# Performance work log

Measured on AMD Instinct MI355X. Metric: run time of the kernel, lower is better.

The kernel has to match this reference:

```python
import jax, jax.numpy as jnp
import numpy as np


def _nearest(x, h, w):
    # torch F.interpolate(mode='nearest'): src_idx = floor(dst_idx * in/out)
    Hi, Wi = x.shape[-2], x.shape[-1]
    ri = (jnp.arange(h) * Hi) // h
    ci = (jnp.arange(w) * Wi) // w
    return jnp.take(jnp.take(x, ri, axis=-2), ci, axis=-1)


def _conv2d(x, wgt, bias):
    y = jax.lax.conv_general_dilated(x, wgt, (1, 1), 'SAME',
                                     dimension_numbers=('NCHW', 'OIHW', 'NCHW'))
    return y + bias.reshape(1, -1, 1, 1)


def setup_inputs() -> dict:
    key = jax.random.key(0)
    ks = jax.random.split(key, 6)
    b, c, ref_n, h, w = 1, 128, 4, 64, 64
    Hv, Wv = 256, 256
    return {
        'feats_t': jax.random.normal(ks[0], (b, c, h, w), jnp.float32),
        'feats_ref': jax.random.normal(ks[1], (b, c, ref_n, h, w), jnp.float32),
        'v_t': jax.random.uniform(ks[2], (b, 1, Hv, Wv), dtype=jnp.float32),
        'v_ref': jax.random.uniform(ks[3], (b, 1, ref_n, Hv, Wv), dtype=jnp.float32),
        'conv1_w': jax.random.normal(ks[4], (1, 1, 3, 3), jnp.float32) * 0.1,
        'conv1_b': jnp.zeros((1,), jnp.float32),
        'conv2_w': jax.random.normal(ks[5], (1, 1, 3, 3), jnp.float32) * 0.1,
        'conv2_b': jnp.zeros((1,), jnp.float32),
    }


def reference(feats_t, feats_ref, v_t, v_ref, conv1_w, conv1_b, conv2_w, conv2_b):
    b, c, ref_n, h, w = feats_ref.shape
    # nearest-resize visibility masks to feature resolution
    vt = _nearest(v_t, h, w)                      # (b, 1, h, w)
    vr = _nearest(v_ref, h, w)                    # (b, 1, ref_n, h, w)
    ft = feats_t * vt                             # (b, c, h, w)
    fr = feats_ref * vr                           # (b, c, ref_n, h, w)
    # cost volume: corr[b,r,q,k] = sum_c ft[b,c,q] * fr[b,c,r,k]
    corr = jnp.einsum('bcq,bcrk->brqk',
                      ft.reshape(b, c, h * w),
                      fr.reshape(b, c, ref_n, h * w))
    corr = corr.reshape(b, ref_n, h, w, h, w)
    # separable 4D conv: 3x3 over (h_ref, w_ref), then 3x3 over (h_t, w_t)
    x = _conv2d(corr.reshape(b * ref_n * h * w, 1, h, w), conv1_w, conv1_b)
    x = x.reshape(b, ref_n, h, w, h, w).transpose(0, 1, 4, 5, 2, 3)
    x = _conv2d(x.reshape(b * ref_n * h * w, 1, h, w), conv2_w, conv2_b)
    corr = x.reshape(b, ref_n, h, w, h, w).transpose(0, 1, 4, 5, 2, 3)
    # softmax3d: joint softmax over (ref_n, h_ref, w_ref) per query location
    m = jnp.max(corr, axis=(1, 4, 5), keepdims=True)
    e = jnp.exp(corr - m)
    corr = e / jnp.sum(e, axis=(1, 4, 5), keepdims=True)
    # weighted aggregation: out[b,c,q] = sum_{r,k} fr[b,c,r,k] * corr[b,r,q,k]
    out = jnp.einsum('bcrk,brqk->bcq',
                     fr.reshape(b, c, ref_n, h * w),
                     corr.reshape(b, ref_n, h * w, h * w))
    return out.reshape(b, c, h, w)
```

## Files before the change

kernel.cpp:

```cpp
#include <hip/hip_runtime.h>
#include <stdint.h>

typedef short bf16x8 __attribute__((ext_vector_type(8)));
typedef float f32x16 __attribute__((ext_vector_type(16)));
typedef unsigned int uint4v __attribute__((ext_vector_type(4)));

#define GAS __attribute__((address_space(1)))
#define LAS __attribute__((address_space(3)))

#define CDIM 128
#define NQ   4096
#define NK   16384
#define QT   128
#define KTILE 64

__device__ __forceinline__ unsigned short f2bf(float f) {
    unsigned int u = __builtin_bit_cast(unsigned int, f);
    u = (u + 0x7fffu + ((u >> 16) & 1u)) >> 16;
    return (unsigned short)u;
}

__device__ __forceinline__ void gload_lds16(const void* g, void* l) {
    __builtin_amdgcn_global_load_lds((const GAS unsigned int*)g, (LAS unsigned int*)l, 16, 0, 0);
}

__device__ __forceinline__ unsigned cvtpk(float a, float b) {
    unsigned r;
    asm("v_cvt_pk_bf16_f32 %0, %1, %2" : "=v"(r) : "v"(a), "v"(b));
    return r;
}

__device__ __forceinline__ void swap32(unsigned& a, unsigned& b) {
    asm("v_permlane32_swap_b32 %0, %1" : "+v"(a), "+v"(b));
}

__global__ void prep_q_kernel(const float* __restrict__ feats_t,
                              const float* __restrict__ v_t,
                              const float* __restrict__ w2,
                              unsigned int* __restrict__ Q32) {
    int idx = blockIdx.x * 256 + threadIdx.x;
    int q = idx & 4095, cp = idx >> 12;
    int y = q >> 6, x = q & 63;
    const float* fb0 = feats_t + (size_t)(cp * 2) * 4096;
    const float* fb1 = fb0 + 4096;
    float wv[9];
#pragma unroll
    for (int i = 0; i < 9; ++i) wv[i] = w2[i];
    float acc0 = 0.f, acc1 = 0.f;
#pragma unroll
    for (int u = 0; u < 3; ++u) {
        int yy = y + u - 1;
        if ((unsigned)yy >= 64u) continue;
#pragma unroll
        for (int v = 0; v < 3; ++v) {
            int xx = x + v - 1;
            if ((unsigned)xx >= 64u) continue;
            float m = wv[u * 3 + v] * v_t[yy * 1024 + xx * 4];
            acc0 += m * fb0[yy * 64 + xx];
            acc1 += m * fb1[yy * 64 + xx];
        }
    }
    Q32[(size_t)q * 64 + cp] = (unsigned)f2bf(acc0) | ((unsigned)f2bf(acc1) << 16);
}

__global__ void prep_p_kernel(const float* __restrict__ feats_ref,
                              const float* __restrict__ v_ref,
                              float* __restrict__ P,
                              unsigned short* __restrict__ Vt2) {
    int idx = blockIdx.x * 256 + threadIdx.x;
    int c = idx >> 14, rk = idx & 16383;
    int r = rk >> 12, k4 = rk & 4095, ky = k4 >> 6, kx = k4 & 63;
    float v = feats_ref[idx] * v_ref[r * 65536 + ky * 1024 + kx * 4];
    P[idx] = v;
    Vt2[(size_t)(rk >> 6) * 8192 + (((rk >> 3) & 7) * 128 + c) * 8 + (rk & 7)] = f2bf(v);
}

__global__ void prep_k2_kernel(const float* __restrict__ P,
                               const float* __restrict__ w1,
                               unsigned int* __restrict__ K32) {
    int idx = blockIdx.x * 256 + threadIdx.x;
    int rk = idx & 16383, cp2 = idx >> 14;
    int r = rk >> 12, k4 = rk & 4095, ky = k4 >> 6, kx = k4 & 63;
    const float* pb0 = P + (size_t)(cp2 * 2) * NK + r * 4096;
    const float* pb1 = pb0 + NK;
    float wv[9];
#pragma unroll
    for (int i = 0; i < 9; ++i) wv[i] = w1[i];
    float acc0 = 0.f, acc1 = 0.f;
#pragma unroll
    for (int u = 0; u < 3; ++u) {
        int yy = ky + u - 1;
        if ((unsigned)yy >= 64u) continue;
#pragma unroll
        for (int v = 0; v < 3; ++v) {
            int xx = kx + v - 1;
            if ((unsigned)xx >= 64u) continue;
            float w = wv[u * 3 + v];
            acc0 += w * pb0[yy * 64 + xx];
            acc1 += w * pb1[yy * 64 + xx];
        }
    }
    int tile = rk >> 6, rw = rk & 63;
    K32[(size_t)tile * 4096 + ((cp2 >> 2) * 64 + rw) * 4 + (cp2 & 3)] =
        (unsigned)f2bf(acc0) | ((unsigned)f2bf(acc1) << 16);
}

template<int KS>
__launch_bounds__(256, 2)
__global__ void attn_kernel(const unsigned short* __restrict__ Qg,
                            const unsigned short* __restrict__ Kt,
                            const unsigned short* __restrict__ Vt2,
                            float* __restrict__ Opart,
                            float* __restrict__ lpart) {
    constexpr int KCHUNK = NK / KS;
    constexpr int NITER = KCHUNK / KTILE;
    __shared__ __align__(16) unsigned short KV[2][2][8192];

    const int tid = threadIdx.x;
    const int wid = tid >> 6;
    const int lane = tid & 63;
    const int l31 = lane & 31;
    const int lh = lane >> 5;
    const int ks = blockIdx.x & (KS - 1);
    const int qt = blockIdx.x / KS;
    const int q0 = qt * QT + wid * 32;
    const int tile0 = ks * (KCHUNK / KTILE);

    bf16x8 qf[8];
#pragma unroll
    for (int s = 0; s < 8; ++s)
        qf[s] = *(const bf16x8*)(Qg + (size_t)(q0 + l31) * CDIM + s * 16 + lh * 8);

    f32x16 accO[4];
#pragma unroll
    for (int u = 0; u < 4; ++u)
#pragma unroll
        for (int r = 0; r < 16; ++r) accO[u][r] = 0.f;
    float l_acc = 0.f;

#define STAGE(nb, tg)                                                             \
    do {                                                                          \
        _Pragma("unroll") for (int j = 0; j < 4; ++j) {                           \
            int mb = (wid * 4 + j) * 64;                                          \
            gload_lds16(Kt + (size_t)(tg) * 8192 + (mb + lane) * 8,               \
                        &KV[(nb)][0][mb * 8]);                                    \
            gload_lds16(Vt2 + (size_t)(tg) * 8192 + (mb + lane) * 8,              \
                        &KV[(nb)][1][mb * 8]);                                    \
        }                                                                         \
    } while (0)

    int cur = 0;
    STAGE(0, tile0);
    asm volatile("s_waitcnt vmcnt(0)" ::: "memory");
    __syncthreads();

#pragma unroll 1
    for (int it = 0; it < NITER; ++it) {
        if (it + 1 < NITER) STAGE(cur ^ 1, tile0 + it + 1);

#pragma unroll
        for (int t = 0; t < 2; ++t) {
            f32x16 S;
#pragma unroll
            for (int r = 0; r < 16; ++r) S[r] = 0.f;
#pragma unroll
            for (int s = 0; s < 8; ++s) {
                bf16x8 kf = *(const bf16x8*)(&KV[cur][0][((s * 2 + lh) * 64 + t * 32 + l31) * 8]);
                S = __builtin_amdgcn_mfma_f32_32x32x16_bf16(kf, qf[s], S, 0, 0, 0);
            }
            float p[16];
#pragma unroll
            for (int r = 0; r < 16; ++r) { p[r] = __expf(S[r]); l_acc += p[r]; }
            unsigned w0 = cvtpk(p[0], p[1]),   w1 = cvtpk(p[2], p[3]);
            unsigned w2 = cvtpk(p[4], p[5]),   w3 = cvtpk(p[6], p[7]);
            unsigned w4 = cvtpk(p[8], p[9]),   w5 = cvtpk(p[10], p[11]);
            unsigned w6 = cvtpk(p[12], p[13]), w7 = cvtpk(p[14], p[15]);
            swap32(w0, w2);
            swap32(w1, w3);
            swap32(w4, w6);
            swap32(w5, w7);
            bf16x8 pbA = __builtin_bit_cast(bf16x8, (uint4v){w0, w1, w2, w3});
            bf16x8 pbB = __builtin_bit_cast(bf16x8, (uint4v){w4, w5, w6, w7});
#pragma unroll
            for (int u = 0; u < 4; ++u) {
                bf16x8 vfa = *(const bf16x8*)(&KV[cur][1][((t * 4 + lh) * 128 + u * 32 + l31) * 8]);
                accO[u] = __builtin_amdgcn_mfma_f32_32x32x16_bf16(vfa, pbA, accO[u], 0, 0, 0);
                bf16x8 vfb = *(const bf16x8*)(&KV[cur][1][((t * 4 + 2 + lh) * 128 + u * 32 + l31) * 8]);
                accO[u] = __builtin_amdgcn_mfma_f32_32x32x16_bf16(vfb, pbB, accO[u], 0, 0, 0);
            }
        }
        asm volatile("s_waitcnt vmcnt(0)" ::: "memory");
        __syncthreads();
        cur ^= 1;
    }
#undef STAGE

    l_acc += __shfl_xor(l_acc, 32);
    if (lane < 32) lpart[ks * NQ + q0 + l31] = l_acc;
#pragma unroll
    for (int u = 0; u < 4; ++u)
#pragma unroll
        for (int r = 0; r < 16; ++r) {
            int c = u * 32 + (r & 3) + 8 * (r >> 2) + 4 * lh;
            Opart[((size_t)(ks * CDIM + c)) * NQ + q0 + l31] = accO[u][r];
        }
}

template<int KS>
__global__ void reduce_kernel(const float* __restrict__ Opart,
                              const float* __restrict__ lpart,
                              float* __restrict__ out) {
    int i = blockIdx.x * 256 + threadIdx.x;
    int c = i >> 12, q = i & 4095;
    float den = 0.f, o = 0.f;
#pragma unroll
    for (int s = 0; s < KS; ++s) {
        den += lpart[s * NQ + q];
        o += Opart[((size_t)(s * CDIM + c)) * NQ + q];
    }
    out[(size_t)c * NQ + q] = o / den;
}

extern "C" void kernel_launch(void* const* d_in, const int* in_sizes, int n_in,
                              void* d_out, int out_size, void* d_ws, size_t ws_size,
                              hipStream_t stream) {
    (void)in_sizes; (void)n_in; (void)out_size;
    const float* feats_t   = (const float*)d_in[0];
    const float* feats_ref = (const float*)d_in[1];
    const float* v_t       = (const float*)d_in[2];
    const float* v_ref     = (const float*)d_in[3];
    const float* w1        = (const float*)d_in[4];
    const float* w2        = (const float*)d_in[6];
    float* out = (float*)d_out;

    const size_t opart_off = (size_t)(9u << 20);
    const size_t need8  = opart_off + (size_t)8  * NQ * CDIM * 4 + (size_t)8  * NQ * 4;
    const size_t need16 = opart_off + (size_t)16 * NQ * CDIM * 4 + (size_t)16 * NQ * 4;
    if (ws_size < need8) return;
    const bool big = (ws_size >= need16);

    char* ws = (char*)d_ws;
    unsigned int*   Q   = (unsigned int*)(ws);
    unsigned short* Kt  = (unsigned short*)(ws + (size_t)(1u << 20));
    unsigned short* Vt2 = (unsigned short*)(ws + (size_t)(5u << 20));
    float* Opart = (float*)(ws + opart_off);
    float* P     = Opart;

    hipLaunchKernelGGL(prep_q_kernel, dim3(1024), dim3(256), 0, stream, feats_t, v_t, w2, Q);
    hipLaunchKernelGGL(prep_p_kernel, dim3(8192), dim3(256), 0, stream, feats_ref, v_ref, P, Vt2);
    hipLaunchKernelGGL(prep_k2_kernel, dim3(4096), dim3(256), 0, stream, P, w1, (unsigned int*)Kt);
    if (big) {
        float* lpart = (float*)(ws + opart_off + (size_t)16 * NQ * CDIM * 4);
        hipLaunchKernelGGL(HIP_KERNEL_NAME(attn_kernel<16>), dim3((NQ / QT) * 16), dim3(256), 0,
                           stream, (const unsigned short*)Q, Kt, Vt2, Opart, lpart);
        hipLaunchKernelGGL(HIP_KERNEL_NAME(reduce_kernel<16>), dim3(2048), dim3(256), 0,
                           stream, Opart, lpart, out);
    } else {
        float* lpart = (float*)(ws + opart_off + (size_t)8 * NQ * CDIM * 4);
        hipLaunchKernelGGL(HIP_KERNEL_NAME(attn_kernel<8>), dim3((NQ / QT) * 8), dim3(256), 0,
                           stream, (const unsigned short*)Q, Kt, Vt2, Opart, lpart);
        hipLaunchKernelGGL(HIP_KERNEL_NAME(reduce_kernel<8>), dim3(2048), dim3(256), 0,
                           stream, Opart, lpart, out);
    }
}
```

Baseline: 73.08 us.

## Halve K tile to 32, raise occupancy, add 32-way split, use exp2

Shrinks the key tile from 64 to 32 rows and re-lays out the K and V staging buffers to match, halving shared memory per block. Launch bounds go from 2 to 4 blocks per CU to hide latency better. The QK^T product is split into two independent accumulators so the MFMA chains overlap. Q is pre-scaled by log2(e) so the softmax can use exp2f instead of __expf. A 32-way key split is added when the workspace is large enough, which raises parallelism but doubles the partial output traffic the reduce kernel has to read.

Result: slower. 117.0 us (+60.1%).

```diff
diff --git a/kernel.cpp b/kernel.cpp
--- a/kernel.cpp
+++ b/kernel.cpp
@@ -1,5 +1,6 @@
 #include <hip/hip_runtime.h>
 #include <stdint.h>
+#include <math.h>
 
 typedef short bf16x8 __attribute__((ext_vector_type(8)));
 typedef float f32x16 __attribute__((ext_vector_type(16)));
@@ -12,7 +13,8 @@
 #define NQ   4096
 #define NK   16384
 #define QT   128
-#define KTILE 64
+#define KTILE 32
+#define LOG2E 1.4426950408889634f
 
 __device__ __forceinline__ unsigned short f2bf(float f) {
     unsigned int u = __builtin_bit_cast(unsigned int, f);
@@ -60,7 +62,8 @@
             acc1 += m * fb1[yy * 64 + xx];
         }
     }
-    Q32[(size_t)q * 64 + cp] = (unsigned)f2bf(acc0) | ((unsigned)f2bf(acc1) << 16);
+    Q32[(size_t)q * 64 + cp] =
+        (unsigned)f2bf(acc0 * LOG2E) | ((unsigned)f2bf(acc1 * LOG2E) << 16);
 }
 
 __global__ void prep_p_kernel(const float* __restrict__ feats_ref,
@@ -72,7 +75,7 @@
     int r = rk >> 12, k4 = rk & 4095, ky = k4 >> 6, kx = k4 & 63;
     float v = feats_ref[idx] * v_ref[r * 65536 + ky * 1024 + kx * 4];
     P[idx] = v;
-    Vt2[(size_t)(rk >> 6) * 8192 + (((rk >> 3) & 7) * 128 + c) * 8 + (rk & 7)] = f2bf(v);
+    Vt2[(size_t)(rk >> 5) * 4096 + (((rk >> 3) & 3) * 128 + c) * 8 + (rk & 7)] = f2bf(v);
 }
 
 __global__ void prep_k2_kernel(const float* __restrict__ P,
@@ -100,21 +103,20 @@
             acc1 += w * pb1[yy * 64 + xx];
         }
     }
-    int tile = rk >> 6, rw = rk & 63;
-    K32[(size_t)tile * 4096 + ((cp2 >> 2) * 64 + rw) * 4 + (cp2 & 3)] =
+    int tile = rk >> 5, rw = rk & 31;
+    K32[(size_t)tile * 2048 + ((cp2 >> 2) * 32 + rw) * 4 + (cp2 & 3)] =
         (unsigned)f2bf(acc0) | ((unsigned)f2bf(acc1) << 16);
 }
 
 template<int KS>
-__launch_bounds__(256, 2)
+__launch_bounds__(256, 4)
 __global__ void attn_kernel(const unsigned short* __restrict__ Qg,
                             const unsigned short* __restrict__ Kt,
                             const unsigned short* __restrict__ Vt2,
                             float* __restrict__ Opart,
                             float* __restrict__ lpart) {
-    constexpr int KCHUNK = NK / KS;
-    constexpr int NITER = KCHUNK / KTILE;
-    __shared__ __align__(16) unsigned short KV[2][2][8192];
+    constexpr int NITER = (NK / KS) / KTILE;
+    __shared__ __align__(16) unsigned short KV[2][2][4096];
 
     const int tid = threadIdx.x;
     const int wid = tid >> 6;
@@ -124,7 +126,7 @@
     const int ks = blockIdx.x & (KS - 1);
     const int qt = blockIdx.x / KS;
     const int q0 = qt * QT + wid * 32;
-    const int tile0 = ks * (KCHUNK / KTILE);
+    const int tile0 = ks * NITER;
 
     bf16x8 qf[8];
 #pragma unroll
@@ -140,11 +142,11 @@
 
 #define STAGE(nb, tg)                                                             \
     do {                                                                          \
-        _Pragma("unroll") for (int j = 0; j < 4; ++j) {                           \
-            int mb = (wid * 4 + j) * 64;                                          \
-            gload_lds16(Kt + (size_t)(tg) * 8192 + (mb + lane) * 8,               \
+        _Pragma("unroll") for (int j = 0; j < 2; ++j) {                           \
+            int mb = (wid * 2 + j) * 64;                                          \
+            gload_lds16(Kt + (size_t)(tg) * 4096 + (mb + lane) * 8,               \
                         &KV[(nb)][0][mb * 8]);                                    \
-            gload_lds16(Vt2 + (size_t)(tg) * 8192 + (mb + lane) * 8,              \
+            gload_lds16(Vt2 + (size_t)(tg) * 4096 + (mb + lane) * 8,              \
                         &KV[(nb)][1][mb * 8]);                                    \
         }                                                                         \
     } while (0)
@@ -158,36 +160,41 @@
     for (int it = 0; it < NITER; ++it) {
         if (it + 1 < NITER) STAGE(cur ^ 1, tile0 + it + 1);
 
-#pragma unroll
-        for (int t = 0; t < 2; ++t) {
-            f32x16 S;
-#pragma unroll
-            for (int r = 0; r < 16; ++r) S[r] = 0.f;
-#pragma unroll
-            for (int s = 0; s < 8; ++s) {
-                bf16x8 kf = *(const bf16x8*)(&KV[cur][0][((s * 2 + lh) * 64 + t * 32 + l31) * 8]);
-                S = __builtin_amdgcn_mfma_f32_32x32x16_bf16(kf, qf[s], S, 0, 0, 0);
-            }
-            float p[16];
-#pragma unroll
-            for (int r = 0; r < 16; ++r) { p[r] = __expf(S[r]); l_acc += p[r]; }
-            unsigned w0 = cvtpk(p[0], p[1]),   w1 = cvtpk(p[2], p[3]);
-            unsigned w2 = cvtpk(p[4], p[5]),   w3 = cvtpk(p[6], p[7]);
-            unsigned w4 = cvtpk(p[8], p[9]),   w5 = cvtpk(p[10], p[11]);
-            unsigned w6 = cvtpk(p[12], p[13]), w7 = cvtpk(p[14], p[15]);
-            swap32(w0, w2);
-            swap32(w1, w3);
-            swap32(w4, w6);
-            swap32(w5, w7);
-            bf16x8 pbA = __builtin_bit_cast(bf16x8, (uint4v){w0, w1, w2, w3});
-            bf16x8 pbB = __builtin_bit_cast(bf16x8, (uint4v){w4, w5, w6, w7});
-#pragma unroll
-            for (int u = 0; u < 4; ++u) {
-                bf16x8 vfa = *(const bf16x8*)(&KV[cur][1][((t * 4 + lh) * 128 + u * 32 + l31) * 8]);
-                accO[u] = __builtin_amdgcn_mfma_f32_32x32x16_bf16(vfa, pbA, accO[u], 0, 0, 0);
-                bf16x8 vfb = *(const bf16x8*)(&KV[cur][1][((t * 4 + 2 + lh) * 128 + u * 32 + l31) * 8]);
-                accO[u] = __builtin_amdgcn_mfma_f32_32x32x16_bf16(vfb, pbB, accO[u], 0, 0, 0);
-            }
+        f32x16 Sa, Sb;
+#pragma unroll
+        for (int r = 0; r < 16; ++r) { Sa[r] = 0.f; Sb[r] = 0.f; }
+#pragma unroll
+        for (int s = 0; s < 4; ++s) {
+            bf16x8 kf = *(const bf16x8*)(&KV[cur][0][((s * 2 + lh) * 32 + l31) * 8]);
+            Sa = __builtin_amdgcn_mfma_f32_32x32x16_bf16(kf, qf[s], Sa, 0, 0, 0);
+        }
+#pragma unroll
+        for (int s = 4; s < 8; ++s) {
+            bf16x8 kf = *(const bf16x8*)(&KV[cur][0][((s * 2 + lh) * 32 + l31) * 8]);
+            Sb = __builtin_amdgcn_mfma_f32_32x32x16_bf16(kf, qf[s], Sb, 0, 0, 0);
+        }
+        float p[16];
+#pragma unroll
+        for (int r = 0; r < 16; ++r) {
+            p[r] = exp2f(Sa[r] + Sb[r]);
+            l_acc += p[r];
+        }
+        unsigned w0 = cvtpk(p[0], p[1]),   w1 = cvtpk(p[2], p[3]);
+        unsigned w2 = cvtpk(p[4], p[5]),   w3 = cvtpk(p[6], p[7]);
+        unsigned w4 = cvtpk(p[8], p[9]),   w5 = cvtpk(p[10], p[11]);
+        unsigned w6 = cvtpk(p[12], p[13]), w7 = cvtpk(p[14], p[15]);
+        swap32(w0, w2);
+        swap32(w1, w3);
+        swap32(w4, w6);
+        swap32(w5, w7);
+        bf16x8 pbA = __builtin_bit_cast(bf16x8, (uint4v){w0, w1, w2, w3});
+        bf16x8 pbB = __builtin_bit_cast(bf16x8, (uint4v){w4, w5, w6, w7});
+#pragma unroll
+        for (int u = 0; u < 4; ++u) {
+            bf16x8 vfa = *(const bf16x8*)(&KV[cur][1][((lh) * 128 + u * 32 + l31) * 8]);
+            accO[u] = __builtin_amdgcn_mfma_f32_32x32x16_bf16(vfa, pbA, accO[u], 0, 0, 0);
+            bf16x8 vfb = *(const bf16x8*)(&KV[cur][1][((2 + lh) * 128 + u * 32 + l31) * 8]);
+            accO[u] = __builtin_amdgcn_mfma_f32_32x32x16_bf16(vfb, pbB, accO[u], 0, 0, 0);
         }
         asm volatile("s_waitcnt vmcnt(0)" ::: "memory");
         __syncthreads();
@@ -234,10 +241,11 @@
     float* out = (float*)d_out;
 
     const size_t opart_off = (size_t)(9u << 20);
-    const size_t need8  = opart_off + (size_t)8  * NQ * CDIM * 4 + (size_t)8  * NQ * 4;
-    const size_t need16 = opart_off + (size_t)16 * NQ * CDIM * 4 + (size_t)16 * NQ * 4;
+    const size_t per_split = (size_t)NQ * CDIM * 4;
+    const size_t need32 = opart_off + 32 * per_split + 32 * NQ * 4;
+    const size_t need16 = opart_off + 16 * per_split + 16 * NQ * 4;
+    const size_t need8  = opart_off + 8  * per_split + 8  * NQ * 4;
     if (ws_size < need8) return;
-    const bool big = (ws_size >= need16);
 
     char* ws = (char*)d_ws;
     unsigned int*   Q   = (unsigned int*)(ws);
@@ -249,14 +257,21 @@
     hipLaunchKernelGGL(prep_q_kernel, dim3(1024), dim3(256), 0, stream, feats_t, v_t, w2, Q);
     hipLaunchKernelGGL(prep_p_kernel, dim3(8192), dim3(256), 0, stream, feats_ref, v_ref, P, Vt2);
     hipLaunchKernelGGL(prep_k2_kernel, dim3(4096), dim3(256), 0, stream, P, w1, (unsigned int*)Kt);
-    if (big) {
-        float* lpart = (float*)(ws + opart_off + (size_t)16 * NQ * CDIM * 4);
+
+    if (ws_size >= need32) {
+        float* lpart = (float*)(ws + opart_off + 32 * per_split);
+        hipLaunchKernelGGL(HIP_KERNEL_NAME(attn_kernel<32>), dim3((NQ / QT) * 32), dim3(256), 0,
+                           stream, (const unsigned short*)Q, Kt, Vt2, Opart, lpart);
+        hipLaunchKernelGGL(HIP_KERNEL_NAME(reduce_kernel<32>), dim3(2048), dim3(256), 0,
+                           stream, Opart, lpart, out);
+    } else if (ws_size >= need16) {
+        float* lpart = (float*)(ws + opart_off + 16 * per_split);
         hipLaunchKernelGGL(HIP_KERNEL_NAME(attn_kernel<16>), dim3((NQ / QT) * 16), dim3(256), 0,
                            stream, (const unsigned short*)Q, Kt, Vt2, Opart, lpart);
         hipLaunchKernelGGL(HIP_KERNEL_NAME(reduce_kernel<16>), dim3(2048), dim3(256), 0,
                            stream, Opart, lpart, out);
     } else {
-        float* lpart = (float*)(ws + opart_off + (size_t)8 * NQ * CDIM * 4);
+        float* lpart = (float*)(ws + opart_off + 8 * per_split);
         hipLaunchKernelGGL(HIP_KERNEL_NAME(attn_kernel<8>), dim3((NQ / QT) * 8), dim3(256), 0,
                            stream, (const unsigned short*)Q, Kt, Vt2, Opart, lpart);
         hipLaunchKernelGGL(HIP_KERNEL_NAME(reduce_kernel<8>), dim3(2048), dim3(256), 0,
```

## Split each key tile across two wave groups and fold log2e into Q

Applied to the files above, without the earlier changes.

The attention kernel now launches 512 threads per block. Two groups of four waves each handle half of every 64-key tile for the same 32-query strips, and their partial O and l accumulators are combined through LDS at the end. Q is prescaled by log2e at prep time so the inner loop can call exp2f instead of __expf. The barrier now sits at the top of each iteration so the prefetch is issued after the sync. This adds more waves per CU and shorter per-wave dependency chains, at the cost of an extra LDS reduction and higher register pressure under launch_bounds(512,4).

Result: slower. 89.15 us (+22.0%).

```diff
diff --git a/kernel.cpp b/kernel.cpp
--- a/kernel.cpp
+++ b/kernel.cpp
@@ -1,5 +1,6 @@
 #include <hip/hip_runtime.h>
 #include <stdint.h>
+#include <math.h>
 
 typedef short bf16x8 __attribute__((ext_vector_type(8)));
 typedef float f32x16 __attribute__((ext_vector_type(16)));
@@ -13,6 +14,7 @@
 #define NK   16384
 #define QT   128
 #define KTILE 64
+#define LOG2E 1.4426950408889634f
 
 __device__ __forceinline__ unsigned short f2bf(float f) {
     unsigned int u = __builtin_bit_cast(unsigned int, f);
@@ -60,7 +62,8 @@
             acc1 += m * fb1[yy * 64 + xx];
         }
     }
-    Q32[(size_t)q * 64 + cp] = (unsigned)f2bf(acc0) | ((unsigned)f2bf(acc1) << 16);
+    Q32[(size_t)q * 64 + cp] =
+        (unsigned)f2bf(acc0 * LOG2E) | ((unsigned)f2bf(acc1 * LOG2E) << 16);
 }
 
 __global__ void prep_p_kernel(const float* __restrict__ feats_ref,
@@ -106,25 +109,27 @@
 }
 
 template<int KS>
-__launch_bounds__(256, 2)
+__launch_bounds__(512, 4)
 __global__ void attn_kernel(const unsigned short* __restrict__ Qg,
                             const unsigned short* __restrict__ Kt,
                             const unsigned short* __restrict__ Vt2,
                             float* __restrict__ Opart,
                             float* __restrict__ lpart) {
-    constexpr int KCHUNK = NK / KS;
-    constexpr int NITER = KCHUNK / KTILE;
+    constexpr int NITER = (NK / KS) / KTILE;
     __shared__ __align__(16) unsigned short KV[2][2][8192];
+    __shared__ float lred[4][32];
 
     const int tid = threadIdx.x;
     const int wid = tid >> 6;
     const int lane = tid & 63;
     const int l31 = lane & 31;
     const int lh = lane >> 5;
+    const int strip = wid & 3;
+    const int h = wid >> 2;
     const int ks = blockIdx.x & (KS - 1);
     const int qt = blockIdx.x / KS;
-    const int q0 = qt * QT + wid * 32;
-    const int tile0 = ks * (KCHUNK / KTILE);
+    const int q0 = qt * QT + strip * 32;
+    const int tile0 = ks * NITER;
 
     bf16x8 qf[8];
 #pragma unroll
@@ -140,8 +145,8 @@
 
 #define STAGE(nb, tg)                                                             \
     do {                                                                          \
-        _Pragma("unroll") for (int j = 0; j < 4; ++j) {                           \
-            int mb = (wid * 4 + j) * 64;                                          \
+        _Pragma("unroll") for (int j = 0; j < 2; ++j) {                           \
+            int mb = (wid * 2 + j) * 64;                                          \
             gload_lds16(Kt + (size_t)(tg) * 8192 + (mb + lane) * 8,               \
                         &KV[(nb)][0][mb * 8]);                                    \
             gload_lds16(Vt2 + (size_t)(tg) * 8192 + (mb + lane) * 8,              \
@@ -151,59 +156,72 @@
 
     int cur = 0;
     STAGE(0, tile0);
-    asm volatile("s_waitcnt vmcnt(0)" ::: "memory");
-    __syncthreads();
 
 #pragma unroll 1
     for (int it = 0; it < NITER; ++it) {
-        if (it + 1 < NITER) STAGE(cur ^ 1, tile0 + it + 1);
-
-#pragma unroll
-        for (int t = 0; t < 2; ++t) {
-            f32x16 S;
-#pragma unroll
-            for (int r = 0; r < 16; ++r) S[r] = 0.f;
-#pragma unroll
-            for (int s = 0; s < 8; ++s) {
-                bf16x8 kf = *(const bf16x8*)(&KV[cur][0][((s * 2 + lh) * 64 + t * 32 + l31) * 8]);
-                S = __builtin_amdgcn_mfma_f32_32x32x16_bf16(kf, qf[s], S, 0, 0, 0);
-            }
-            float p[16];
-#pragma unroll
-            for (int r = 0; r < 16; ++r) { p[r] = __expf(S[r]); l_acc += p[r]; }
-            unsigned w0 = cvtpk(p[0], p[1]),   w1 = cvtpk(p[2], p[3]);
-            unsigned w2 = cvtpk(p[4], p[5]),   w3 = cvtpk(p[6], p[7]);
-            unsigned w4 = cvtpk(p[8], p[9]),   w5 = cvtpk(p[10], p[11]);
-            unsigned w6 = cvtpk(p[12], p[13]), w7 = cvtpk(p[14], p[15]);
-            swap32(w0, w2);
-            swap32(w1, w3);
-            swap32(w4, w6);
-            swap32(w5, w7);
-            bf16x8 pbA = __builtin_bit_cast(bf16x8, (uint4v){w0, w1, w2, w3});
-            bf16x8 pbB = __builtin_bit_cast(bf16x8, (uint4v){w4, w5, w6, w7});
-#pragma unroll
-            for (int u = 0; u < 4; ++u) {
-                bf16x8 vfa = *(const bf16x8*)(&KV[cur][1][((t * 4 + lh) * 128 + u * 32 + l31) * 8]);
-                accO[u] = __builtin_amdgcn_mfma_f32_32x32x16_bf16(vfa, pbA, accO[u], 0, 0, 0);
-                bf16x8 vfb = *(const bf16x8*)(&KV[cur][1][((t * 4 + 2 + lh) * 128 + u * 32 + l31) * 8]);
-                accO[u] = __builtin_amdgcn_mfma_f32_32x32x16_bf16(vfb, pbB, accO[u], 0, 0, 0);
-            }
-        }
         asm volatile("s_waitcnt vmcnt(0)" ::: "memory");
         __syncthreads();
+        if (it + 1 < NITER) STAGE(cur ^ 1, tile0 + it + 1);
+
+        f32x16 S;
+#pragma unroll
+        for (int r = 0; r < 16; ++r) S[r] = 0.f;
+#pragma unroll
+        for (int s = 0; s < 8; ++s) {
+            bf16x8 kf = *(const bf16x8*)(&KV[cur][0][((s * 2 + lh) * 64 + h * 32 + l31) * 8]);
+            S = __builtin_amdgcn_mfma_f32_32x32x16_bf16(kf, qf[s], S, 0, 0, 0);
+        }
+        float p[16];
+#pragma unroll
+        for (int r = 0; r < 16; ++r) { p[r] = exp2f(S[r]); l_acc += p[r]; }
+        unsigned w0 = cvtpk(p[0], p[1]),   w1 = cvtpk(p[2], p[3]);
+        unsigned w2 = cvtpk(p[4], p[5]),   w3 = cvtpk(p[6], p[7]);
+        unsigned w4 = cvtpk(p[8], p[9]),   w5 = cvtpk(p[10], p[11]);
+        unsigned w6 = cvtpk(p[12], p[13]), w7 = cvtpk(p[14], p[15]);
+        swap32(w0, w2);
+        swap32(w1, w3);
+        swap32(w4, w6);
+        swap32(w5, w7);
+        bf16x8 pbA = __builtin_bit_cast(bf16x8, (uint4v){w0, w1, w2, w3});
+        bf16x8 pbB = __builtin_bit_cast(bf16x8, (uint4v){w4, w5, w6, w7});
+#pragma unroll
+        for (int u = 0; u < 4; ++u) {
+            bf16x8 vfa = *(const bf16x8*)(&KV[cur][1][((h * 4 + lh) * 128 + u * 32 + l31) * 8]);
+            accO[u] = __builtin_amdgcn_mfma_f32_32x32x16_bf16(vfa, pbA, accO[u], 0, 0, 0);
+            bf16x8 vfb = *(const bf16x8*)(&KV[cur][1][((h * 4 + 2 + lh) * 128 + u * 32 + l31) * 8]);
+            accO[u] = __builtin_amdgcn_mfma_f32_32x32x16_bf16(vfb, pbB, accO[u], 0, 0, 0);
+        }
         cur ^= 1;
     }
 #undef STAGE
 
+    __syncthreads();
+    float* mbuf = (float*)&KV[0][0][0];
     l_acc += __shfl_xor(l_acc, 32);
-    if (lane < 32) lpart[ks * NQ + q0 + l31] = l_acc;
-#pragma unroll
-    for (int u = 0; u < 4; ++u)
-#pragma unroll
-        for (int r = 0; r < 16; ++r) {
-            int c = u * 32 + (r & 3) + 8 * (r >> 2) + 4 * lh;
-            Opart[((size_t)(ks * CDIM + c)) * NQ + q0 + l31] = accO[u][r];
-        }
+    if (h == 1) {
+        float* sb = mbuf + strip * 4096;
+#pragma unroll
+        for (int u = 0; u < 4; ++u)
+#pragma unroll
+            for (int r = 0; r < 16; ++r) {
+                int c = u * 32 + (r & 3) + 8 * (r >> 2) + 4 * lh;
+                sb[c * 32 + l31] = accO[u][r];
+            }
+        if (lane < 32) lred[strip][l31] = l_acc;
+    }
+    __syncthreads();
+    if (h == 0) {
+        float* sb = mbuf + strip * 4096;
+        float lt = l_acc + lred[strip][l31];
+        if (lane < 32) lpart[ks * NQ + q0 + l31] = lt;
+#pragma unroll
+        for (int u = 0; u < 4; ++u)
+#pragma unroll
+            for (int r = 0; r < 16; ++r) {
+                int c = u * 32 + (r & 3) + 8 * (r >> 2) + 4 * lh;
+                Opart[((size_t)(ks * CDIM + c)) * NQ + q0 + l31] = accO[u][r] + sb[c * 32 + l31];
+            }
+    }
 }
 
 template<int KS>
@@ -234,10 +252,10 @@
     float* out = (float*)d_out;
 
     const size_t opart_off = (size_t)(9u << 20);
-    const size_t need8  = opart_off + (size_t)8  * NQ * CDIM * 4 + (size_t)8  * NQ * 4;
-    const size_t need16 = opart_off + (size_t)16 * NQ * CDIM * 4 + (size_t)16 * NQ * 4;
+    const size_t per_split = (size_t)NQ * CDIM * 4;
+    const size_t need16 = opart_off + 16 * per_split + 16 * NQ * 4;
+    const size_t need8  = opart_off + 8  * per_split + 8  * NQ * 4;
     if (ws_size < need8) return;
-    const bool big = (ws_size >= need16);
 
     char* ws = (char*)d_ws;
     unsigned int*   Q   = (unsigned int*)(ws);
@@ -249,15 +267,16 @@
     hipLaunchKernelGGL(prep_q_kernel, dim3(1024), dim3(256), 0, stream, feats_t, v_t, w2, Q);
     hipLaunchKernelGGL(prep_p_kernel, dim3(8192), dim3(256), 0, stream, feats_ref, v_ref, P, Vt2);
     hipLaunchKernelGGL(prep_k2_kernel, dim3(4096), dim3(256), 0, stream, P, w1, (unsigned int*)Kt);
-    if (big) {
-        float* lpart = (float*)(ws + opart_off + (size_t)16 * NQ * CDIM * 4);
-        hipLaunchKernelGGL(HIP_KERNEL_NAME(attn_kernel<16>), dim3((NQ / QT) * 16), dim3(256), 0,
+
+    if (ws_size >= need16) {
+        float* lpart = (float*)(ws + opart_off + 16 * per_split);
+        hipLaunchKernelGGL(HIP_KERNEL_NAME(attn_kernel<16>), dim3((NQ / QT) * 16), dim3(512), 0,
                            stream, (const unsigned short*)Q, Kt, Vt2, Opart, lpart);
         hipLaunchKernelGGL(HIP_KERNEL_NAME(reduce_kernel<16>), dim3(2048), dim3(256), 0,
                            stream, Opart, lpart, out);
     } else {
-        float* lpart = (float*)(ws + opart_off + (size_t)8 * NQ * CDIM * 4);
-        hipLaunchKernelGGL(HIP_KERNEL_NAME(attn_kernel<8>), dim3((NQ / QT) * 8), dim3(256), 0,
+        float* lpart = (float*)(ws + opart_off + 8 * per_split);
+        hipLaunchKernelGGL(HIP_KERNEL_NAME(attn_kernel<8>), dim3((NQ / QT) * 8), dim3(512), 0,
                            stream, (const unsigned short*)Q, Kt, Vt2, Opart, lpart);
         hipLaunchKernelGGL(HIP_KERNEL_NAME(reduce_kernel<8>), dim3(2048), dim3(256), 0,
                            stream, Opart, lpart, out);
```
